# Kernel optimization log

Measured on AMD Instinct MI355X. Metric: run time of the kernel, lower is better.

The kernel has to match this reference:

```python
import jax, jax.numpy as jnp
import numpy as np

B, S, H = 4, 2048, 1024
NH, HD = 16, 64
FF = 4 * H
EPS = 1e-5


def _layernorm(x, g, b):
    m = jnp.mean(x, axis=-1, keepdims=True)
    v = jnp.mean((x - m) ** 2, axis=-1, keepdims=True)
    return (x - m) * jax.lax.rsqrt(v + EPS) * g + b


def setup_inputs() -> dict:
    key = jax.random.key(0)
    ks = jax.random.split(key, 12)
    std = 1.0 / np.sqrt(H)
    inp = {
        "x": jax.random.normal(ks[0], (B, S, H), dtype=jnp.float32),
        "attention_mask": jnp.ones((B, S), dtype=bool),
        "Wq": jax.random.normal(ks[1], (H, H), dtype=jnp.float32) * std,
        "bq": jnp.zeros((H,), dtype=jnp.float32),
        "Wk": jax.random.normal(ks[2], (H, H), dtype=jnp.float32) * std,
        "bk": jnp.zeros((H,), dtype=jnp.float32),
        "Wv": jax.random.normal(ks[3], (H, H), dtype=jnp.float32) * std,
        "bv": jnp.zeros((H,), dtype=jnp.float32),
        "Wo": jax.random.normal(ks[4], (H, H), dtype=jnp.float32) * std,
        "bo": jnp.zeros((H,), dtype=jnp.float32),
        "g1": jnp.ones((H,), dtype=jnp.float32),
        "b1": jnp.zeros((H,), dtype=jnp.float32),
        "g2": jnp.ones((H,), dtype=jnp.float32),
        "b2": jnp.zeros((H,), dtype=jnp.float32),
        "Wm1": jax.random.normal(ks[5], (FF, H), dtype=jnp.float32) * std,
        "bm1": jnp.zeros((FF,), dtype=jnp.float32),
        "Wm2": jax.random.normal(ks[6], (H, FF), dtype=jnp.float32) * (1.0 / np.sqrt(FF)),
        "bm2": jnp.zeros((H,), dtype=jnp.float32),
    }
    return inp


def reference(x, attention_mask, Wq, bq, Wk, bk, Wv, bv, Wo, bo,
              g1, b1, g2, b2, Wm1, bm1, Wm2, bm2):
    scale = 1.0 / np.sqrt(HD)
    normed = _layernorm(x, g1, b1)
    # torch Linear: y = x @ W.T + b
    q = (normed @ Wq.T + bq).reshape(B, S, NH, HD)
    k = (normed @ Wk.T + bk).reshape(B, S, NH, HD)
    v = (normed @ Wv.T + bv).reshape(B, S, NH, HD)
    # scores: [B, NH, S, S]
    scores = jnp.einsum("bqhd,bkhd->bhqk", q, k) * scale
    scores = jnp.where(attention_mask[:, None, None, :], scores, -jnp.inf)
    attn = jax.nn.softmax(scores, axis=-1)
    out = jnp.einsum("bhqk,bkhd->bqhd", attn, v).reshape(B, S, H)
    out = out @ Wo.T + bo
    x = x + out
    h = _layernorm(x, g2, b2)
    h = jax.nn.gelu(h @ Wm1.T + bm1, approximate=False) @ Wm2.T + bm2
    return x + h
```

## Files before the change

### kernel.cpp

```cpp
#include <hip/hip_runtime.h>
#include <math.h>


typedef unsigned short u16;
typedef unsigned int   u32;
typedef __attribute__((ext_vector_type(4)))  float f32x4;
typedef __attribute__((ext_vector_type(16))) float f32x16;
typedef __attribute__((ext_vector_type(8)))  short short8;
typedef __attribute__((ext_vector_type(4)))  short short4v;

__device__ __forceinline__ u16 f2bf(float f){
  union { float f; u32 u; } v; v.f = f;
  u32 u = v.u;
  return (u16)((u + 0x7fffu + ((u >> 16) & 1u)) >> 16);
}
__device__ __forceinline__ float bf2f(u16 h){
  union { u32 u; float f; } v; v.u = ((u32)h) << 16;
  return v.f;
}

__device__ __forceinline__ void async16(const u16* g, u16* l){
  __builtin_amdgcn_global_load_lds((const __attribute__((address_space(1))) u32*)g,
                                   (__attribute__((address_space(3))) u32*)l, 16, 0, 0);
}

__device__ __forceinline__ u32 cvt_pk_bf16(float lo, float hi){
  u32 r;
  asm("v_cvt_pk_bf16_f32 %0, %1, %2" : "=v"(r) : "v"(lo), "v"(hi));
  return r;
}

__device__ __forceinline__ short8 frag4(u32 a, u32 b, u32 c, u32 d){
  union { u32 u[4]; short8 s; } x;
  x.u[0] = a; x.u[1] = b; x.u[2] = c; x.u[3] = d;
  return x.s;
}

__global__ __launch_bounds__(256) void k_cvt_all(
    const float* __restrict__ Wq, const float* __restrict__ Wk,
    const float* __restrict__ Wv, const float* __restrict__ Wo,
    const float* __restrict__ Wm1, const float* __restrict__ Wm2,
    const float* __restrict__ bq, const float* __restrict__ bk,
    const float* __restrict__ bv,
    u16* __restrict__ wqkv, u16* __restrict__ wo,
    u16* __restrict__ wm1, u16* __restrict__ wm2, float* __restrict__ bqkv){
  int c = blockIdx.x * 256 + threadIdx.x;
  const float* src; u16* dst;
  if      (c <  262144){ src = Wq  + c*4;             dst = wqkv + c*4; }
  else if (c <  524288){ src = Wk  + (c-262144)*4;    dst = wqkv + 1048576 + (c-262144)*4; }
  else if (c <  786432){ src = Wv  + (c-524288)*4;    dst = wqkv + 2097152 + (c-524288)*4; }
  else if (c < 1048576){ src = Wo  + (c-786432)*4;    dst = wo  + (c-786432)*4; }
  else if (c < 2097152){ src = Wm1 + (c-1048576)*4;   dst = wm1 + (c-1048576)*4; }
  else if (c < 3145728){ src = Wm2 + (c-2097152)*4;   dst = wm2 + (c-2097152)*4; }
  else if (c < 3146496){
    int i = (c - 3145728)*4;
    const float* bsrc = i < 1024 ? bq + i : (i < 2048 ? bk + i - 1024 : bv + i - 2048);
    *(float4*)(bqkv + i) = *(const float4*)bsrc;
    return;
  } else return;
  float4 v = *(const float4*)src;
  ushort4 o; o.x = f2bf(v.x); o.y = f2bf(v.y); o.z = f2bf(v.z); o.w = f2bf(v.w);
  *(ushort4*)dst = o;
}

__global__ __launch_bounds__(256) void k_ln(const float* __restrict__ x,
                                            const float* __restrict__ g,
                                            const float* __restrict__ b,
                                            u16* __restrict__ out){
  int row = blockIdx.x;
  int t = threadIdx.x;
  const float* xr = x + (size_t)row * 1024;
  float4 v = ((const float4*)xr)[t];
  float s = v.x + v.y + v.z + v.w;
  float q = v.x*v.x + v.y*v.y + v.z*v.z + v.w*v.w;
  #pragma unroll
  for (int off = 1; off < 64; off <<= 1){
    s += __shfl_xor(s, off);
    q += __shfl_xor(q, off);
  }
  __shared__ float ps[4], pq[4];
  int w = t >> 6, l = t & 63;
  if (l == 0){ ps[w] = s; pq[w] = q; }
  __syncthreads();
  s = ps[0] + ps[1] + ps[2] + ps[3];
  q = pq[0] + pq[1] + pq[2] + pq[3];
  float mean = s * (1.0f/1024.0f);
  float var  = q * (1.0f/1024.0f) - mean*mean;
  float rstd = rsqrtf(var + 1e-5f);
  float4 gv = ((const float4*)g)[t];
  float4 bv = ((const float4*)b)[t];
  ushort4 o;
  o.x = f2bf((v.x - mean)*rstd*gv.x + bv.x);
  o.y = f2bf((v.y - mean)*rstd*gv.y + bv.y);
  o.z = f2bf((v.z - mean)*rstd*gv.z + bv.z);
  o.w = f2bf((v.w - mean)*rstd*gv.w + bv.w);
  ((ushort4*)(out + (size_t)row * 1024))[t] = o;
}

#define MF(FRB, FCB) { \
  _Pragma("unroll") for (int ks = 0; ks < 2; ks++) \
  _Pragma("unroll") for (int fr = 0; fr < 4; fr++) \
  _Pragma("unroll") for (int fc = 0; fc < 2; fc++) \
    acc[(FRB)+fr][(FCB)+fc] = __builtin_amdgcn_mfma_f32_16x16x32_bf16( \
        a[fr][ks], b[fc][ks], acc[(FRB)+fr][(FCB)+fc], 0, 0, 0); }

#define STAGE(BUF, H, KT) { \
  async16(hbase[H] + (size_t)gr_[0]*K + (KT)*64 + gc_[0], &lds[BUF][H][t*8]); \
  async16(hbase[H] + (size_t)gr_[1]*K + (KT)*64 + gc_[1], &lds[BUF][H][4096 + t*8]); }

#define BARRIER() { __builtin_amdgcn_s_barrier(); __builtin_amdgcn_sched_barrier(0); }

template<int EPI>
__global__ __launch_bounds__(512, 2) void k_gemm256(const u16* __restrict__ A,
    const u16* __restrict__ Bw, const float* __restrict__ bias, void* __restrict__ Cp,
    const float* __restrict__ res, int M, int N, int K, int ntn){
  __shared__ __align__(16) u16 lds[2][4][8192];
  const int t = threadIdx.x;
  const int l = t & 63, w = t >> 6;
  const int wm = w >> 2, wn = w & 3;
  const int lr = l & 15, g = l >> 4;

  const int nwg = gridDim.x;
  int wg = blockIdx.x;
  if (!(nwg & 7)) wg = (wg & 7) * (nwg >> 3) + (wg >> 3);
  const int bm = (wg / ntn) * 256, bn = (wg % ntn) * 256;

  int gr_[2], gc_[2];
  #pragma unroll
  for (int i = 0; i < 2; i++){
    int ch = i*512 + t;
    int sr = ch >> 7, sc = (ch >> 6) & 1, r = (ch >> 2) & 15;
    int c  = ((ch & 3) * 8) ^ (((r >> 3) & 1) << 4);
    gr_[i] = sr*16 + r;
    gc_[i] = sc*32 + c;
  }
  const u16* hbase[4] = { A  + (size_t) bm        * K,
                          A  + (size_t)(bm + 128) * K,
                          Bw + (size_t) bn        * K,
                          Bw + (size_t)(bn + 128) * K };

  const int roff = lr*32 + ((g*8) ^ (((lr >> 3) & 1) << 4));

  f32x4 acc[8][4];
  #pragma unroll
  for (int i = 0; i < 8; i++)
    #pragma unroll
    for (int j = 0; j < 4; j++)
      acc[i][j] = (f32x4)(0.0f);
  short8 a[4][2], b[2][2];

  #define LDA(HB) { _Pragma("unroll") for (int fr = 0; fr < 4; fr++) \
    _Pragma("unroll") for (int ks = 0; ks < 2; ks++) \
      a[fr][ks] = *(const short8*)((HB) + (fr*4 + wm*2 + ks)*512 + roff); }
  #define LDB(HB) { _Pragma("unroll") for (int fc = 0; fc < 2; fc++) \
    _Pragma("unroll") for (int ks = 0; ks < 2; ks++) \
      b[fc][ks] = *(const short8*)((HB) + ((fc*4 + wn)*2 + ks)*512 + roff); }

  const int NT = K >> 6;
  STAGE(0, 0, 0); STAGE(0, 2, 0); STAGE(0, 3, 0); STAGE(0, 1, 0);
  asm volatile("s_waitcnt vmcnt(4)" ::: "memory");
  BARRIER();

  for (int kt = 0; kt < NT; kt++){
    const int cu = kt & 1, nx = cu ^ 1;
    const u16* LA0 = lds[cu][0]; const u16* LA1 = lds[cu][1];
    const u16* LB0 = lds[cu][2]; const u16* LB1 = lds[cu][3];
    const bool pf = (kt + 1 < NT);
    LDA(LA0); LDB(LB0);
    if (pf) STAGE(nx, 0, kt+1);
    __builtin_amdgcn_s_setprio(1);
    MF(0, 0);
    __builtin_amdgcn_s_setprio(0);
    if (pf) asm volatile("s_waitcnt vmcnt(4)" ::: "memory");
    else    asm volatile("s_waitcnt vmcnt(2)" ::: "memory");
    BARRIER();
    LDB(LB1);
    if (pf) STAGE(nx, 2, kt+1);
    __builtin_amdgcn_s_setprio(1);
    MF(0, 2);
    __builtin_amdgcn_s_setprio(0);
    if (pf) asm volatile("s_waitcnt vmcnt(4)" ::: "memory");
    else    asm volatile("s_waitcnt vmcnt(0)" ::: "memory");
    BARRIER();
    LDA(LA1);
    if (pf) STAGE(nx, 3, kt+1);
    __builtin_amdgcn_s_setprio(1);
    MF(4, 2);
    __builtin_amdgcn_s_setprio(0);
    BARRIER();
    LDB(LB0);
    if (pf) STAGE(nx, 1, kt+1);
    __builtin_amdgcn_s_setprio(1);
    MF(4, 0);
    __builtin_amdgcn_s_setprio(0);
    if (pf) asm volatile("s_waitcnt vmcnt(4)" ::: "memory");
    BARRIER();
  }

  const int m0 = bm + wm*16 + g*4;
  const int n0 = bn + wn*16 + lr;
  #pragma unroll
  for (int fc = 0; fc < 4; fc++){
    int col = n0 + fc*64;
    float bb = bias[col];
    #pragma unroll
    for (int fr = 0; fr < 8; fr++){
      int rowb = m0 + fr*32;
      #pragma unroll
      for (int r = 0; r < 4; r++){
        float v = acc[fr][fc][r] + bb;
        if constexpr (EPI == 2)
          v = 0.5f * v * (1.0f + erff(v * 0.70710678118654752f));
        size_t idx = (size_t)(rowb + r) * N + col;
        if constexpr (EPI == 1)
          ((float*)Cp)[idx] = v + res[idx];
        else
          ((u16*)Cp)[idx] = f2bf(v);
      }
    }
  }
}
#undef MF
#undef STAGE
#undef LDA
#undef LDB
#undef BARRIER

__global__ __launch_bounds__(512) void k_flash(const u16* __restrict__ QKV,
                                               u16* __restrict__ O){
  constexpr int QSTR = 3072, OSTR = 1024;
  __shared__ __align__(16) u16 lK [2][64*64];
  __shared__ __align__(16) u16 lVT[2][64*64];

  const int t = threadIdx.x;
  const int l = t & 63, w = t >> 6;
  const int c31 = l & 31, h = l >> 5;
  const int rbx = ((blockIdx.x & 7) << 6) + (blockIdx.x >> 3);
  const int qt = rbx & 7, bh = rbx >> 3;
  const size_t rowbase = (size_t)(bh >> 4) * 2048;
  const int hd = (bh & 15) * 64;
  const u16* Qg = QKV + rowbase * QSTR + hd;
  const u16* Kg = Qg + 1024;
  const u16* Vg = Qg + 2048;
  u16* Og = O + rowbase * OSTR + hd;
  const int qrow0 = qt * 256 + w * 32;

  short8 qf[4];
  #pragma unroll
  for (int d0 = 0; d0 < 4; d0++){
    short8 v = *(const short8*)(Qg + (size_t)(qrow0 + c31) * QSTR + d0*16 + 8*h);
    #pragma unroll
    for (int j = 0; j < 8; j++)
      v[j] = (short)f2bf(bf2f((u16)v[j]) * 0.18033688011112042f);
    qf[d0] = v;
  }

  f32x16 oa0 = (f32x16)(0.0f), oa1 = (f32x16)(0.0f);
  float m_run = -1e30f, l_run = 0.0f;

  const int vkv0 = 2*(t & 31), vdh = t >> 5;
  const int rb = (c31 & 7) << 4;

  {
    int row = t >> 3, c = (t & 7) ^ (row & 7);
    async16(Kg + (size_t)row * QSTR + c*8, &lK[0][t*8]);
    const u16* vs = Vg + (size_t)vkv0 * QSTR + vdh*4;
    short4v v0 = *(const short4v*)(vs);
    short4v v1 = *(const short4v*)(vs + QSTR);
    #pragma unroll
    for (int j = 0; j < 4; j++){
      int d = vdh*4 + j;
      u32 word = (u32)(u16)v0[j] | ((u32)(u16)v1[j] << 16);
      *(u32*)((char*)&lVT[0][0] + d*128 + ((vkv0*2) ^ ((d&7)<<4))) = word;
    }
  }
  __syncthreads();

  short4v v0s, v1s;
  for (int kt = 0; kt < 32; kt++){
    const int cur = kt & 1;
    const char* lKc = (const char*)&lK[cur][0];
    const char* lVc = (const char*)&lVT[cur][0];

    if (kt < 31){
      int row = t >> 3, c = (t & 7) ^ (row & 7);
      async16(Kg + (size_t)((kt+1)*64 + row) * QSTR + c*8, &lK[cur^1][t*8]);
      const u16* vs = Vg + (size_t)((kt+1)*64 + vkv0) * QSTR + vdh*4;
      v0s = *(const short4v*)(vs);
      v1s = *(const short4v*)(vs + QSTR);
    }

    f32x16 sa0 = (f32x16)(0.0f), sa1 = (f32x16)(0.0f);
    __builtin_amdgcn_s_setprio(1);
    #pragma unroll
    for (int d0 = 0; d0 < 4; d0++){
      int cb = (d0*32 + 16*h) ^ rb;
      short8 kf0 = *(const short8*)(lKc + c31*128 + cb);
      short8 kf1 = *(const short8*)(lKc + (32+c31)*128 + cb);
      sa0 = __builtin_amdgcn_mfma_f32_32x32x16_bf16(kf0, qf[d0], sa0, 0, 0, 0);
      sa1 = __builtin_amdgcn_mfma_f32_32x32x16_bf16(kf1, qf[d0], sa1, 0, 0, 0);
    }
    __builtin_amdgcn_s_setprio(0);

    float pm = fmaxf(sa0[0], sa0[1]);
    #pragma unroll
    for (int r = 2; r < 16; r++) pm = fmaxf(pm, sa0[r]);
    #pragma unroll
    for (int r = 0; r < 16; r++) pm = fmaxf(pm, sa1[r]);
    pm = fmaxf(pm, __shfl_xor(pm, 32));
    if (!__all(pm <= m_run + 8.0f)){
      float mnew = fmaxf(m_run, pm);
      float alpha = exp2f(m_run - mnew);
      m_run = mnew;
      l_run *= alpha;
      #pragma unroll
      for (int r = 0; r < 16; r++){
        int qr = (r&3) + 8*(r>>2) + 4*h;
        float ar = __shfl(alpha, qr);
        oa0[r] *= ar; oa1[r] *= ar;
      }
    }
    float rs = 0.0f;
    #pragma unroll
    for (int r = 0; r < 16; r++){ float p = exp2f(sa0[r] - m_run); sa0[r] = p; rs += p; }
    #pragma unroll
    for (int r = 0; r < 16; r++){ float p = exp2f(sa1[r] - m_run); sa1[r] = p; rs += p; }
    rs += __shfl_xor(rs, 32);
    l_run += rs;

    short8 pa[4];
    {
      u32 a0 = cvt_pk_bf16(sa0[0], sa0[1]),  a1 = cvt_pk_bf16(sa0[2], sa0[3]);
      u32 a2 = cvt_pk_bf16(sa0[4], sa0[5]),  a3 = cvt_pk_bf16(sa0[6], sa0[7]);
      asm("v_permlane32_swap_b32 %0, %1" : "+v"(a0), "+v"(a2));
      asm("v_permlane32_swap_b32 %0, %1" : "+v"(a1), "+v"(a3));
      pa[0] = frag4(a0, a1, a2, a3);
      u32 b0 = cvt_pk_bf16(sa0[8], sa0[9]),  b1 = cvt_pk_bf16(sa0[10], sa0[11]);
      u32 b2 = cvt_pk_bf16(sa0[12], sa0[13]), b3 = cvt_pk_bf16(sa0[14], sa0[15]);
      asm("v_permlane32_swap_b32 %0, %1" : "+v"(b0), "+v"(b2));
      asm("v_permlane32_swap_b32 %0, %1" : "+v"(b1), "+v"(b3));
      pa[1] = frag4(b0, b1, b2, b3);
      u32 c0 = cvt_pk_bf16(sa1[0], sa1[1]),  c1 = cvt_pk_bf16(sa1[2], sa1[3]);
      u32 c2 = cvt_pk_bf16(sa1[4], sa1[5]),  c3 = cvt_pk_bf16(sa1[6], sa1[7]);
      asm("v_permlane32_swap_b32 %0, %1" : "+v"(c0), "+v"(c2));
      asm("v_permlane32_swap_b32 %0, %1" : "+v"(c1), "+v"(c3));
      pa[2] = frag4(c0, c1, c2, c3);
      u32 d0 = cvt_pk_bf16(sa1[8], sa1[9]),  d1 = cvt_pk_bf16(sa1[10], sa1[11]);
      u32 d2 = cvt_pk_bf16(sa1[12], sa1[13]), d3 = cvt_pk_bf16(sa1[14], sa1[15]);
      asm("v_permlane32_swap_b32 %0, %1" : "+v"(d0), "+v"(d2));
      asm("v_permlane32_swap_b32 %0, %1" : "+v"(d1), "+v"(d3));
      pa[3] = frag4(d0, d1, d2, d3);
    }

    __builtin_amdgcn_s_setprio(1);
    #pragma unroll
    for (int ks = 0; ks < 4; ks++){
      int cb = (ks*32 + 16*h) ^ rb;
      short8 vb0 = *(const short8*)(lVc + c31*128 + cb);
      short8 vb1 = *(const short8*)(lVc + (32+c31)*128 + cb);
      oa0 = __builtin_amdgcn_mfma_f32_32x32x16_bf16(pa[ks], vb0, oa0, 0, 0, 0);
      oa1 = __builtin_amdgcn_mfma_f32_32x32x16_bf16(pa[ks], vb1, oa1, 0, 0, 0);
    }
    __builtin_amdgcn_s_setprio(0);

    if (kt < 31){
      #pragma unroll
      for (int j = 0; j < 4; j++){
        int d = vdh*4 + j;
        u32 word = (u32)(u16)v0s[j] | ((u32)(u16)v1s[j] << 16);
        *(u32*)((char*)&lVT[cur^1][0] + d*128 + ((vkv0*2) ^ ((d&7)<<4))) = word;
      }
    }
    __syncthreads();
  }

  float linv = 1.0f / l_run;
  #pragma unroll
  for (int r = 0; r < 16; r++){
    int qr = (r&3) + 8*(r>>2) + 4*h;
    float lr2 = __shfl(linv, qr);
    size_t ro = (size_t)(qrow0 + qr) * OSTR;
    Og[ro + c31]      = f2bf(oa0[r] * lr2);
    Og[ro + 32 + c31] = f2bf(oa1[r] * lr2);
  }
}

extern "C" void kernel_launch(void* const* d_in, const int* in_sizes, int n_in,
                              void* d_out, int out_size, void* d_ws, size_t ws_size,
                              hipStream_t stream){
  const float* x   = (const float*)d_in[0];
  const float* Wq  = (const float*)d_in[2];
  const float* bq  = (const float*)d_in[3];
  const float* Wk  = (const float*)d_in[4];
  const float* bk  = (const float*)d_in[5];
  const float* Wv  = (const float*)d_in[6];
  const float* bv  = (const float*)d_in[7];
  const float* Wo  = (const float*)d_in[8];
  const float* bo  = (const float*)d_in[9];
  const float* g1  = (const float*)d_in[10];
  const float* b1  = (const float*)d_in[11];
  const float* g2  = (const float*)d_in[12];
  const float* b2  = (const float*)d_in[13];
  const float* Wm1 = (const float*)d_in[14];
  const float* bm1 = (const float*)d_in[15];
  const float* Wm2 = (const float*)d_in[16];
  const float* bm2 = (const float*)d_in[17];

  const size_t MB = 1024 * 1024;
  char* ws = (char*)d_ws;
  u16*   wqkv = (u16*)(ws + 0*MB);
  u16*   wo   = (u16*)(ws + 6*MB);
  u16*   wm1  = (u16*)(ws + 8*MB);
  u16*   wm2  = (u16*)(ws + 16*MB);
  float* bqkv = (float*)(ws + 24*MB);
  u16*   nrm  = (u16*)(ws + 25*MB);
  u16*   qkvb = (u16*)(ws + 41*MB);
  u16*   attn = (u16*)(ws + 89*MB);
  float* x2   = (float*)(ws + 105*MB);
  u16*   h1   = (u16*)(ws + 41*MB);

  k_cvt_all<<<12291, 256, 0, stream>>>(Wq, Wk, Wv, Wo, Wm1, Wm2, bq, bk, bv,
                                       wqkv, wo, wm1, wm2, bqkv);

  const int M = 8192;
  k_ln<<<M, 256, 0, stream>>>(x, g1, b1, nrm);
  k_gemm256<0><<<dim3(32*12), 512, 0, stream>>>(nrm, wqkv, bqkv, qkvb, nullptr, M, 3072, 1024, 12);
  k_flash<<<512, 512, 0, stream>>>(qkvb, attn);
  k_gemm256<1><<<dim3(32*4), 512, 0, stream>>>(attn, wo, bo, x2, x, M, 1024, 1024, 4);
  k_ln<<<M, 256, 0, stream>>>(x2, g2, b2, nrm);
  k_gemm256<2><<<dim3(32*16), 512, 0, stream>>>(nrm, wm1, bm1, h1, nullptr, M, 4096, 1024, 16);
  k_gemm256<1><<<dim3(32*4), 512, 0, stream>>>(h1, wm2, bm2, d_out, x2, M, 1024, 4096, 4);
}
```

Before: 474.1 us.

## Add 128x256 GEMM tile variant and halve flash-attention block size for more CTAs

Adds a k_gemm128 kernel with 128-row tiles, used for the QKV, output-projection and MLP-down GEMMs, so those launches have more workgroups (768 and 256 instead of 384 and 128) to fill the CUs better. Flash attention now uses 256-thread blocks covering 128 query rows, with 1024 blocks, and each thread loads twice as much K/V. The XCD-aware block remap in flash is dropped. In exchange, each GEMM tile reuses the B operand less, and K/V tiles are reloaded by twice as many attention blocks.

Result: faster. 421.7 us (-11.0%).

```diff
diff --git a/kernel.cpp b/kernel.cpp
--- a/kernel.cpp
+++ b/kernel.cpp
@@ -7,7 +7,6 @@
 typedef __attribute__((ext_vector_type(4)))  float f32x4;
 typedef __attribute__((ext_vector_type(16))) float f32x16;
 typedef __attribute__((ext_vector_type(8)))  short short8;
-typedef __attribute__((ext_vector_type(4)))  short short4v;
 
 __device__ __forceinline__ u16 f2bf(float f){
   union { float f; u32 u; } v; v.f = f;
@@ -110,6 +109,27 @@
 
 #define BARRIER() { __builtin_amdgcn_s_barrier(); __builtin_amdgcn_sched_barrier(0); }
 
+#define STAGE_DECODE() \
+  int gr_[2], gc_[2]; \
+  _Pragma("unroll") \
+  for (int i = 0; i < 2; i++){ \
+    int ch = i*512 + t; \
+    int sr = ch >> 7, sc = (ch >> 6) & 1, r = (ch >> 2) & 15; \
+    int c  = ((ch & 3) * 8) ^ (((r >> 3) & 1) << 4); \
+    gr_[i] = sr*16 + r; \
+    gc_[i] = sc*32 + c; \
+  }
+
+#define EPILOG_STORE() { \
+  float v = acc[fr][fc][r] + bb; \
+  if constexpr (EPI == 2) \
+    v = 0.5f * v * (1.0f + erff(v * 0.70710678118654752f)); \
+  size_t idx = (size_t)(rowb + r) * N + col; \
+  if constexpr (EPI == 1) \
+    ((float*)Cp)[idx] = v + res[idx]; \
+  else \
+    ((u16*)Cp)[idx] = f2bf(v); }
+
 template<int EPI>
 __global__ __launch_bounds__(512, 2) void k_gemm256(const u16* __restrict__ A,
     const u16* __restrict__ Bw, const float* __restrict__ bias, void* __restrict__ Cp,
@@ -125,15 +145,7 @@
   if (!(nwg & 7)) wg = (wg & 7) * (nwg >> 3) + (wg >> 3);
   const int bm = (wg / ntn) * 256, bn = (wg % ntn) * 256;
 
-  int gr_[2], gc_[2];
-  #pragma unroll
-  for (int i = 0; i < 2; i++){
-    int ch = i*512 + t;
-    int sr = ch >> 7, sc = (ch >> 6) & 1, r = (ch >> 2) & 15;
-    int c  = ((ch & 3) * 8) ^ (((r >> 3) & 1) << 4);
-    gr_[i] = sr*16 + r;
-    gc_[i] = sc*32 + c;
-  }
+  STAGE_DECODE();
   const u16* hbase[4] = { A  + (size_t) bm        * K,
                           A  + (size_t)(bm + 128) * K,
                           Bw + (size_t) bn        * K,
@@ -207,26 +219,105 @@
     for (int fr = 0; fr < 8; fr++){
       int rowb = m0 + fr*32;
       #pragma unroll
-      for (int r = 0; r < 4; r++){
-        float v = acc[fr][fc][r] + bb;
-        if constexpr (EPI == 2)
-          v = 0.5f * v * (1.0f + erff(v * 0.70710678118654752f));
-        size_t idx = (size_t)(rowb + r) * N + col;
-        if constexpr (EPI == 1)
-          ((float*)Cp)[idx] = v + res[idx];
-        else
-          ((u16*)Cp)[idx] = f2bf(v);
-      }
-    }
-  }
+      for (int r = 0; r < 4; r++) EPILOG_STORE();
+    }
+  }
+  #undef LDA
+  #undef LDB
+}
+
+template<int EPI>
+__global__ __launch_bounds__(512, 2) void k_gemm128(const u16* __restrict__ A,
+    const u16* __restrict__ Bw, const float* __restrict__ bias, void* __restrict__ Cp,
+    const float* __restrict__ res, int M, int N, int K, int ntn){
+  __shared__ __align__(16) u16 lds[2][3][8192];
+  const int t = threadIdx.x;
+  const int l = t & 63, w = t >> 6;
+  const int wm = w >> 2, wn = w & 3;
+  const int lr = l & 15, g = l >> 4;
+
+  const int nwg = gridDim.x;
+  int wg = blockIdx.x;
+  if (!(nwg & 7)) wg = (wg & 7) * (nwg >> 3) + (wg >> 3);
+  const int bm = (wg / ntn) * 128, bn = (wg % ntn) * 256;
+
+  STAGE_DECODE();
+  const u16* hbase[3] = { A  + (size_t) bm        * K,
+                          Bw + (size_t) bn        * K,
+                          Bw + (size_t)(bn + 128) * K };
+
+  const int roff = lr*32 + ((g*8) ^ (((lr >> 3) & 1) << 4));
+
+  f32x4 acc[4][4];
+  #pragma unroll
+  for (int i = 0; i < 4; i++)
+    #pragma unroll
+    for (int j = 0; j < 4; j++)
+      acc[i][j] = (f32x4)(0.0f);
+  short8 a[4][2], b[2][2];
+
+  #define LDA(HB) { _Pragma("unroll") for (int fr = 0; fr < 4; fr++) \
+    _Pragma("unroll") for (int ks = 0; ks < 2; ks++) \
+      a[fr][ks] = *(const short8*)((HB) + (fr*4 + wm*2 + ks)*512 + roff); }
+  #define LDB(HB) { _Pragma("unroll") for (int fc = 0; fc < 2; fc++) \
+    _Pragma("unroll") for (int ks = 0; ks < 2; ks++) \
+      b[fc][ks] = *(const short8*)((HB) + ((fc*4 + wn)*2 + ks)*512 + roff); }
+  #define MF128(FCB) { \
+    _Pragma("unroll") for (int ks = 0; ks < 2; ks++) \
+    _Pragma("unroll") for (int fr = 0; fr < 4; fr++) \
+    _Pragma("unroll") for (int fc = 0; fc < 2; fc++) \
+      acc[fr][(FCB)+fc] = __builtin_amdgcn_mfma_f32_16x16x32_bf16( \
+          a[fr][ks], b[fc][ks], acc[fr][(FCB)+fc], 0, 0, 0); }
+
+  const int NT = K >> 6;
+  STAGE(0, 0, 0); STAGE(0, 1, 0); STAGE(0, 2, 0);
+  asm volatile("s_waitcnt vmcnt(2)" ::: "memory");
+  BARRIER();
+
+  for (int kt = 0; kt < NT; kt++){
+    const int cu = kt & 1, nx = cu ^ 1;
+    const bool pf = (kt + 1 < NT);
+    LDA(lds[cu][0]); LDB(lds[cu][1]);
+    if (pf){ STAGE(nx, 0, kt+1); STAGE(nx, 1, kt+1); }
+    __builtin_amdgcn_s_setprio(1);
+    MF128(0);
+    __builtin_amdgcn_s_setprio(0);
+    if (pf) asm volatile("s_waitcnt vmcnt(4)" ::: "memory");
+    else    asm volatile("s_waitcnt vmcnt(0)" ::: "memory");
+    BARRIER();
+    LDB(lds[cu][2]);
+    if (pf) STAGE(nx, 2, kt+1);
+    __builtin_amdgcn_s_setprio(1);
+    MF128(2);
+    __builtin_amdgcn_s_setprio(0);
+    if (pf) asm volatile("s_waitcnt vmcnt(2)" ::: "memory");
+    BARRIER();
+  }
+
+  const int m0 = bm + wm*16 + g*4;
+  const int n0 = bn + wn*16 + lr;
+  #pragma unroll
+  for (int fc = 0; fc < 4; fc++){
+    int col = n0 + fc*64;
+    float bb = bias[col];
+    #pragma unroll
+    for (int fr = 0; fr < 4; fr++){
+      int rowb = m0 + fr*32;
+      #pragma unroll
+      for (int r = 0; r < 4; r++) EPILOG_STORE();
+    }
+  }
+  #undef LDA
+  #undef LDB
+  #undef MF128
 }
 #undef MF
 #undef STAGE
-#undef LDA
-#undef LDB
 #undef BARRIER
-
-__global__ __launch_bounds__(512) void k_flash(const u16* __restrict__ QKV,
+#undef STAGE_DECODE
+#undef EPILOG_STORE
+
+__global__ __launch_bounds__(256) void k_flash(const u16* __restrict__ QKV,
                                                u16* __restrict__ O){
   constexpr int QSTR = 3072, OSTR = 1024;
   __shared__ __align__(16) u16 lK [2][64*64];
@@ -235,15 +326,15 @@
   const int t = threadIdx.x;
   const int l = t & 63, w = t >> 6;
   const int c31 = l & 31, h = l >> 5;
-  const int rbx = ((blockIdx.x & 7) << 6) + (blockIdx.x >> 3);
-  const int qt = rbx & 7, bh = rbx >> 3;
+  const int bx = blockIdx.x;
+  const int qt = bx & 15, bh = bx >> 4;
   const size_t rowbase = (size_t)(bh >> 4) * 2048;
   const int hd = (bh & 15) * 64;
   const u16* Qg = QKV + rowbase * QSTR + hd;
   const u16* Kg = Qg + 1024;
   const u16* Vg = Qg + 2048;
   u16* Og = O + rowbase * OSTR + hd;
-  const int qrow0 = qt * 256 + w * 32;
+  const int qrow0 = qt * 128 + w * 32;
 
   short8 qf[4];
   #pragma unroll
@@ -262,32 +353,40 @@
   const int rb = (c31 & 7) << 4;
 
   {
-    int row = t >> 3, c = (t & 7) ^ (row & 7);
-    async16(Kg + (size_t)row * QSTR + c*8, &lK[0][t*8]);
-    const u16* vs = Vg + (size_t)vkv0 * QSTR + vdh*4;
-    short4v v0 = *(const short4v*)(vs);
-    short4v v1 = *(const short4v*)(vs + QSTR);
-    #pragma unroll
-    for (int j = 0; j < 4; j++){
-      int d = vdh*4 + j;
-      u32 word = (u32)(u16)v0[j] | ((u32)(u16)v1[j] << 16);
+    #pragma unroll
+    for (int i = 0; i < 2; i++){
+      int idx = i*256 + t;
+      int row = idx >> 3, c = (idx & 7) ^ (row & 7);
+      async16(Kg + (size_t)row * QSTR + c*8, &lK[0][idx*8]);
+    }
+    const u16* vs = Vg + (size_t)vkv0 * QSTR + vdh*8;
+    short8 v0 = *(const short8*)(vs);
+    short8 v1 = *(const short8*)(vs + QSTR);
+    #pragma unroll
+    for (int i = 0; i < 8; i++){
+      int d = vdh*8 + i;
+      u32 word = (u32)(u16)v0[i] | ((u32)(u16)v1[i] << 16);
       *(u32*)((char*)&lVT[0][0] + d*128 + ((vkv0*2) ^ ((d&7)<<4))) = word;
     }
   }
   __syncthreads();
 
-  short4v v0s, v1s;
+  short8 v0s, v1s;
   for (int kt = 0; kt < 32; kt++){
     const int cur = kt & 1;
     const char* lKc = (const char*)&lK[cur][0];
     const char* lVc = (const char*)&lVT[cur][0];
 
     if (kt < 31){
-      int row = t >> 3, c = (t & 7) ^ (row & 7);
-      async16(Kg + (size_t)((kt+1)*64 + row) * QSTR + c*8, &lK[cur^1][t*8]);
-      const u16* vs = Vg + (size_t)((kt+1)*64 + vkv0) * QSTR + vdh*4;
-      v0s = *(const short4v*)(vs);
-      v1s = *(const short4v*)(vs + QSTR);
+      #pragma unroll
+      for (int i = 0; i < 2; i++){
+        int idx = i*256 + t;
+        int row = idx >> 3, c = (idx & 7) ^ (row & 7);
+        async16(Kg + (size_t)((kt+1)*64 + row) * QSTR + c*8, &lK[cur^1][idx*8]);
+      }
+      const u16* vs = Vg + (size_t)((kt+1)*64 + vkv0) * QSTR + vdh*8;
+      v0s = *(const short8*)(vs);
+      v1s = *(const short8*)(vs + QSTR);
     }
 
     f32x16 sa0 = (f32x16)(0.0f), sa1 = (f32x16)(0.0f);
@@ -365,9 +464,9 @@
 
     if (kt < 31){
       #pragma unroll
-      for (int j = 0; j < 4; j++){
-        int d = vdh*4 + j;
-        u32 word = (u32)(u16)v0s[j] | ((u32)(u16)v1s[j] << 16);
+      for (int i = 0; i < 8; i++){
+        int d = vdh*8 + i;
+        u32 word = (u32)(u16)v0s[i] | ((u32)(u16)v1s[i] << 16);
         *(u32*)((char*)&lVT[cur^1][0] + d*128 + ((vkv0*2) ^ ((d&7)<<4))) = word;
       }
     }
@@ -424,10 +523,10 @@
 
   const int M = 8192;
   k_ln<<<M, 256, 0, stream>>>(x, g1, b1, nrm);
-  k_gemm256<0><<<dim3(32*12), 512, 0, stream>>>(nrm, wqkv, bqkv, qkvb, nullptr, M, 3072, 1024, 12);
-  k_flash<<<512, 512, 0, stream>>>(qkvb, attn);
-  k_gemm256<1><<<dim3(32*4), 512, 0, stream>>>(attn, wo, bo, x2, x, M, 1024, 1024, 4);
+  k_gemm128<0><<<dim3(64*12), 512, 0, stream>>>(nrm, wqkv, bqkv, qkvb, nullptr, M, 3072, 1024, 12);
+  k_flash<<<1024, 256, 0, stream>>>(qkvb, attn);
+  k_gemm128<1><<<dim3(64*4), 512, 0, stream>>>(attn, wo, bo, x2, x, M, 1024, 1024, 4);
   k_ln<<<M, 256, 0, stream>>>(x2, g2, b2, nrm);
   k_gemm256<2><<<dim3(32*16), 512, 0, stream>>>(nrm, wm1, bm1, h1, nullptr, M, 4096, 1024, 16);
-  k_gemm256<1><<<dim3(32*4), 512, 0, stream>>>(h1, wm2, bm2, d_out, x2, M, 1024, 4096, 4);
-}
+  k_gemm128<1><<<dim3(64*4), 512, 0, stream>>>(h1, wm2, bm2, d_out, x2, M, 1024, 4096, 4);
+}
```
